# Kernel tuning notes

Measured on AMD Instinct MI355X. Metric: run time of the kernel, lower is better.

The kernel has to match this reference:

```python
import jax, jax.numpy as jnp
import numpy as np

NUM_AUTHOR = 16604
NUM_PAPER = 12455
NUM_NODES = NUM_AUTHOR + NUM_PAPER  # 29059
EMBED_DIM = 300
B = 32768          # batch of query nodes
E = 1048576        # total neighbor edges (avg degree 32)


def setup_inputs() -> dict:
    key = jax.random.key(0)
    k1, k2, k3, k4, k5, k6 = jax.random.split(key, 6)
    nodes = jax.random.randint(k1, (B,), 0, NUM_NODES)
    seg = jnp.sort(jax.random.randint(k2, (E,), 0, B))
    neighbors = jax.random.randint(k3, (E,), 0, NUM_NODES)
    embeddings = jax.random.normal(k4, (NUM_NODES, EMBED_DIM), dtype=jnp.float32)
    # linear1: Linear(3*300 -> 300)
    lim = 1.0 / np.sqrt(3 * EMBED_DIM)
    W1 = jax.random.uniform(k5, (EMBED_DIM, 3 * EMBED_DIM), dtype=jnp.float32, minval=-lim, maxval=lim)
    b1 = jax.random.uniform(k6, (EMBED_DIM,), dtype=jnp.float32, minval=-lim, maxval=lim)
    return {"nodes": nodes, "seg": seg, "neighbors": neighbors,
            "embeddings": embeddings, "W1": W1, "b1": b1}


def reference(nodes, seg, neighbors, embeddings, W1, b1):
    # Gather neighbor embeddings: [E, D] (dominant memory traffic)
    nb_emb = embeddings[neighbors]
    # type_1 = same node type as the query node, type_2 = the other type
    same = (neighbors < NUM_AUTHOR) == (nodes[seg] < NUM_AUTHOR)  # [E] bool
    w1 = same.astype(nb_emb.dtype)[:, None]
    w2 = 1.0 - w1
    sum1 = jax.ops.segment_sum(nb_emb * w1, seg, num_segments=B)   # [B, D]
    sum2 = jax.ops.segment_sum(nb_emb * w2, seg, num_segments=B)
    cnt1 = jax.ops.segment_sum(w1[:, 0], seg, num_segments=B)[:, None]  # [B,1]
    cnt2 = jax.ops.segment_sum(w2[:, 0], seg, num_segments=B)[:, None]
    # mean pooling; empty type falls back to ones (as in the torch code)
    t1 = jnp.where(cnt1 > 0, sum1 / jnp.maximum(cnt1, 1.0), 1.0)
    t2 = jnp.where(cnt2 > 0, sum2 / jnp.maximum(cnt2, 1.0), 1.0)
    self_f = embeddings[nodes]  # [B, D]
    combined = jnp.concatenate([self_f, t1, t2], axis=-1)  # [B, 3D]
    return combined @ W1.T + b1  # [B, D]
```

## Files before the change

### kernel.cpp

```cpp
#include <hip/hip_runtime.h>
#include <hip/hip_bf16.h>

#define NUM_AUTHOR 16604
#define EMB_D      300
#define BQ         32768
#define NEDGE      1048576
#define KPAD 960
#define NPAD 320
#define DPAD 320
#define NNODES 29059

#define SEG_BLOCKS 4096
#define PW_BLOCKS  1200
#define CE_BLOCKS  18162

typedef __attribute__((ext_vector_type(8))) short bf16x8;
typedef __attribute__((ext_vector_type(4))) float f32x4;

__device__ __forceinline__ unsigned short f2bf(float f) {
  unsigned int u = __float_as_uint(f);
  u += 0x7fffu + ((u >> 16) & 1u);
  return (unsigned short)(u >> 16);
}

__device__ __forceinline__ void async_copy16(const void* g, void* lds_base) {
  __builtin_amdgcn_global_load_lds(
      (const __attribute__((address_space(1))) unsigned int*)g,
      (__attribute__((address_space(3))) unsigned int*)lds_base, 16, 0, 0);
}

__global__ void prep_all(const int* __restrict__ seg, int* __restrict__ start,
                         const float* __restrict__ W1, unsigned short* __restrict__ Wt,
                         const float* __restrict__ emb, unsigned short* __restrict__ embB) {
  int blk = blockIdx.x;
  if (blk < SEG_BLOCKS) {
    int i = blk * 256 + threadIdx.x;
    int s = seg[i];
    int prev = (i == 0) ? -1 : seg[i - 1];
    if (s != prev) {
      for (int b = prev + 1; b <= s; ++b) start[b] = i;
    }
    if (i == NEDGE - 1) {
      for (int b = s + 1; b <= BQ; ++b) start[b] = NEDGE;
    }
  } else if (blk < SEG_BLOCKS + PW_BLOCKS) {
    int i = (blk - SEG_BLOCKS) * 256 + threadIdx.x;
    int n = i / KPAD, k = i % KPAD;
    int sec = k / 320, kk = k % 320;
    unsigned short v = 0;
    if (n < 300 && kk < 300) v = f2bf(W1[n * 900 + sec * 300 + kk]);
    Wt[i] = v;
  } else {
    int i = (blk - SEG_BLOCKS - PW_BLOCKS) * 256 + threadIdx.x;
    if (i >= NNODES * (DPAD / 2)) return;
    int r = i / (DPAD / 2), cu = i % (DPAD / 2);
    int c = 2 * cu;
    unsigned int lo = 0, hi = 0;
    if (c < EMB_D)     lo = f2bf(emb[(size_t)r * EMB_D + c]);
    if (c + 1 < EMB_D) hi = f2bf(emb[(size_t)r * EMB_D + c + 1]);
    ((unsigned int*)embB)[i] = lo | (hi << 16);
  }
}

__device__ __forceinline__ void accum8(uint4 p, int bit,
                                       float2* atot, float2* a1) {
  unsigned int pk[4] = {p.x, p.y, p.z, p.w};
  float2 v[4];
  #pragma unroll
  for (int k = 0; k < 4; ++k) {
    v[k].x = __uint_as_float(pk[k] << 16);
    v[k].y = __uint_as_float(pk[k] & 0xffff0000u);
  }
  #pragma unroll
  for (int k = 0; k < 4; ++k) {
    atot[k].x += v[k].x; atot[k].y += v[k].y;
  }
  if (__builtin_amdgcn_readfirstlane(bit)) {
    #pragma unroll
    for (int k = 0; k < 4; ++k) {
      a1[k].x += v[k].x; a1[k].y += v[k].y;
    }
  }
}

__global__ __launch_bounds__(128) void pool(
    const int* __restrict__ nodes, const int* __restrict__ neighbors,
    const int* __restrict__ start, const unsigned short* __restrict__ embB,
    unsigned short* __restrict__ comb) {
  int b = blockIdx.x * 2 + (threadIdx.x >> 6);
  int l = threadIdx.x & 63;
  int s0 = start[b], s1 = start[b + 1];
  int node = nodes[b];
  int qa = (node < NUM_AUTHOR) ? 1 : 0;
  bool act = (l < 40);
  const unsigned short* ep = embB + 8 * l;

  float2 atot[4], a1[4];
  #pragma unroll
  for (int k = 0; k < 4; ++k) {
    atot[k] = make_float2(0.f, 0.f);
    a1[k]   = make_float2(0.f, 0.f);
  }
  int c1 = 0;
  int rem = s1 - s0;

  for (int base = 0; base < rem; base += 64) {
    int cl = min(64, rem - base);
    int idx = neighbors[s0 + base + min(l, cl - 1)];
    int same = (((idx < NUM_AUTHOR) ? 1 : 0) == qa) ? 1 : 0;
    unsigned long long bal = __ballot(same != 0);
    unsigned long long msk = (cl >= 64) ? ~0ull : ((1ull << cl) - 1ull);
    c1 += __popcll(bal & msk);
    int off = idx * DPAD;

    int j2 = 0;
    for (; j2 + 8 <= cl; j2 += 8) {
      int o[8];
      #pragma unroll
      for (int q = 0; q < 8; ++q) o[q] = __shfl(off, j2 + q);
      if (act) {
        uint4 p[8];
        #pragma unroll
        for (int q = 0; q < 8; ++q) p[q] = *(const uint4*)(ep + o[q]);
        #pragma unroll
        for (int q = 0; q < 8; ++q)
          accum8(p[q], (int)((bal >> (j2 + q)) & 1), atot, a1);
      }
    }
    for (; j2 < cl; ++j2) {
      int o = __shfl(off, j2);
      if (act) {
        uint4 p = *(const uint4*)(ep + o);
        accum8(p, (int)((bal >> j2) & 1), atot, a1);
      }
    }
  }

  int c2 = rem - c1;
  if (!act) return;

  uint4 selfv = *(const uint4*)(embB + (size_t)node * DPAD + 8 * l);
  float r1 = c1 ? 1.0f / (float)c1 : 0.0f;
  float r2 = c2 ? 1.0f / (float)c2 : 0.0f;
  unsigned int o1[4], o2[4];
  #pragma unroll
  for (int k = 0; k < 4; ++k) {
    float t1lo = c1 ? a1[k].x * r1 : 1.0f;
    float t1hi = c1 ? a1[k].y * r1 : 1.0f;
    float t2lo = c2 ? (atot[k].x - a1[k].x) * r2 : 1.0f;
    float t2hi = c2 ? (atot[k].y - a1[k].y) * r2 : 1.0f;
    o1[k] = (unsigned int)f2bf(t1lo) | ((unsigned int)f2bf(t1hi) << 16);
    o2[k] = (unsigned int)f2bf(t2lo) | ((unsigned int)f2bf(t2hi) << 16);
  }
  uint4* crow = (uint4*)(comb + (size_t)b * KPAD);
  crow[l]      = selfv;
  crow[40 + l] = (uint4){o1[0], o1[1], o1[2], o1[3]};
  crow[80 + l] = (uint4){o2[0], o2[1], o2[2], o2[3]};
}

__global__ __launch_bounds__(256) void gemm(
    const unsigned short* __restrict__ A,
    const unsigned short* __restrict__ Bt,
    const float* __restrict__ b1,
    float* __restrict__ out) {
  __shared__ __align__(16) unsigned short As[64 * 96];
  __shared__ __align__(16) unsigned short Bs[160 * 96];

  int tid  = threadIdx.x;
  int lane = tid & 63;
  int w    = tid >> 6;
  int quad = lane >> 4;
  int l16  = lane & 15;
  int bm = blockIdx.x >> 1;
  int bn = blockIdx.x & 1;
  int wm = w >> 1, wn = w & 1;

  f32x4 acc[2][5];
  for (int i = 0; i < 2; ++i)
    for (int j = 0; j < 5; ++j)
      acc[i][j] = (f32x4){0.f, 0.f, 0.f, 0.f};

  const size_t Abase = (size_t)bm * 64 * KPAD;
  const size_t Bbase = (size_t)bn * 160 * KPAD;

  for (int kt = 0; kt < KPAD / 96; ++kt) {
    int k0 = kt * 96;
    __syncthreads();
    for (int c = w; c < 12; c += 4) {
      int flat = c * 64 + lane;
      int row = flat / 12, kq = flat % 12;
      const unsigned short* g = A + Abase + (size_t)row * KPAD + k0 + kq * 8;
      async_copy16(g, (char*)As + c * 1024);
    }
    for (int c = w; c < 30; c += 4) {
      int flat = c * 64 + lane;
      int nrow = flat / 12, kq = flat % 12;
      const unsigned short* g = Bt + Bbase + (size_t)nrow * KPAD + k0 + kq * 8;
      async_copy16(g, (char*)Bs + c * 1024);
    }
    __syncthreads();

    #pragma unroll
    for (int ks = 0; ks < 3; ++ks) {
      bf16x8 af[2], bf[5];
      for (int rt = 0; rt < 2; ++rt)
        af[rt] = *(const bf16x8*)&As[(wm * 32 + rt * 16 + l16) * 96 + ks * 32 + quad * 8];
      for (int ct = 0; ct < 5; ++ct)
        bf[ct] = *(const bf16x8*)&Bs[(wn * 80 + ct * 16 + l16) * 96 + ks * 32 + quad * 8];
      for (int rt = 0; rt < 2; ++rt)
        for (int ct = 0; ct < 5; ++ct)
          acc[rt][ct] = __builtin_amdgcn_mfma_f32_16x16x32_bf16(
              af[rt], bf[ct], acc[rt][ct], 0, 0, 0);
    }
  }

  int m0 = bm * 64 + wm * 32;
  int n0 = bn * 160 + wn * 80;
  for (int ct = 0; ct < 5; ++ct) {
    int n = n0 + ct * 16 + l16;
    if (n >= 300) continue;
    float bias = b1[n];
    for (int rt = 0; rt < 2; ++rt) {
      int m = m0 + rt * 16 + quad * 4;
      for (int r = 0; r < 4; ++r)
        out[(size_t)(m + r) * 300 + n] = acc[rt][ct][r] + bias;
    }
  }
}

__global__ __launch_bounds__(128) void pool_f32(
    const int* __restrict__ nodes, const int* __restrict__ neighbors,
    const int* __restrict__ start, const float* __restrict__ emb,
    unsigned short* __restrict__ comb) {
  int b = blockIdx.x;
  int t = threadIdx.x;
  if (t >= 80) return;
  int s0 = start[b], s1 = start[b + 1];
  int node = nodes[b];
  int qa = (node < NUM_AUTHOR) ? 1 : 0;
  bool act = (t < 75);
  float a1x = 0.f, a1y = 0.f, a1z = 0.f, a1w = 0.f;
  float a2x = 0.f, a2y = 0.f, a2z = 0.f, a2w = 0.f;
  int c1 = 0;
  #pragma unroll 2
  for (int j = s0; j < s1; ++j) {
    int nb = neighbors[j];
    int fl = (((nb < NUM_AUTHOR) ? 1 : 0) == qa) ? 1 : 0;
    c1 += fl;
    if (act) {
      const float4 v = *(const float4*)(emb + (size_t)nb * EMB_D + 4 * t);
      float w = fl ? 1.0f : 0.0f;
      float u = 1.0f - w;
      a1x += w * v.x; a1y += w * v.y; a1z += w * v.z; a1w += w * v.w;
      a2x += u * v.x; a2y += u * v.y; a2z += u * v.z; a2w += u * v.w;
    }
  }
  int c2 = (s1 - s0) - c1;
  unsigned int ps0 = 0, ps1 = 0, p10 = 0, p11 = 0, p20 = 0, p21 = 0;
  if (act) {
    const float4 sv = *(const float4*)(emb + (size_t)node * EMB_D + 4 * t);
    float r1 = c1 ? 1.0f / (float)c1 : 0.0f;
    float r2 = c2 ? 1.0f / (float)c2 : 0.0f;
    float t1x = c1 ? a1x * r1 : 1.0f, t1y = c1 ? a1y * r1 : 1.0f;
    float t1z = c1 ? a1z * r1 : 1.0f, t1w = c1 ? a1w * r1 : 1.0f;
    float t2x = c2 ? a2x * r2 : 1.0f, t2y = c2 ? a2y * r2 : 1.0f;
    float t2z = c2 ? a2z * r2 : 1.0f, t2w = c2 ? a2w * r2 : 1.0f;
    ps0 = (unsigned int)f2bf(sv.x) | ((unsigned int)f2bf(sv.y) << 16);
    ps1 = (unsigned int)f2bf(sv.z) | ((unsigned int)f2bf(sv.w) << 16);
    p10 = (unsigned int)f2bf(t1x) | ((unsigned int)f2bf(t1y) << 16);
    p11 = (unsigned int)f2bf(t1z) | ((unsigned int)f2bf(t1w) << 16);
    p20 = (unsigned int)f2bf(t2x) | ((unsigned int)f2bf(t2y) << 16);
    p21 = (unsigned int)f2bf(t2z) | ((unsigned int)f2bf(t2w) << 16);
  }
  unsigned int* crow = (unsigned int*)(comb + (size_t)b * KPAD);
  crow[2 * t]       = ps0;  crow[2 * t + 1]       = ps1;
  crow[160 + 2 * t] = p10;  crow[160 + 2 * t + 1] = p11;
  crow[320 + 2 * t] = p20;  crow[320 + 2 * t + 1] = p21;
}

__global__ void seg_bounds_only(const int* __restrict__ seg, int* __restrict__ start) {
  int i = blockIdx.x * 256 + threadIdx.x;
  if (i >= NEDGE) return;
  int s = seg[i];
  int prev = (i == 0) ? -1 : seg[i - 1];
  if (s != prev) for (int b = prev + 1; b <= s; ++b) start[b] = i;
  if (i == NEDGE - 1) for (int b = s + 1; b <= BQ; ++b) start[b] = NEDGE;
}
__global__ void prep_w_only(const float* __restrict__ W1, unsigned short* __restrict__ Wt) {
  int i = blockIdx.x * 256 + threadIdx.x;
  if (i >= NPAD * KPAD) return;
  int n = i / KPAD, k = i % KPAD;
  int sec = k / 320, kk = k % 320;
  unsigned short v = 0;
  if (n < 300 && kk < 300) v = f2bf(W1[n * 900 + sec * 300 + kk]);
  Wt[i] = v;
}

extern "C" void kernel_launch(void* const* d_in, const int* in_sizes, int n_in,
                              void* d_out, int out_size, void* d_ws, size_t ws_size,
                              hipStream_t stream) {
  const int* nodes     = (const int*)d_in[0];
  const int* seg       = (const int*)d_in[1];
  const int* neighbors = (const int*)d_in[2];
  const float* emb     = (const float*)d_in[3];
  const float* W1      = (const float*)d_in[4];
  const float* b1      = (const float*)d_in[5];
  float* out           = (float*)d_out;

  char* ws = (char*)d_ws;
  int* start           = (int*)ws;
  unsigned short* Wt   = (unsigned short*)(ws + 131584);
  unsigned short* comb = (unsigned short*)(ws + 746496);
  unsigned short* embB = (unsigned short*)(ws + 63661056);
  const size_t WS_NEEDED = 82258816;

  if (ws_size >= WS_NEEDED) {
    prep_all<<<SEG_BLOCKS + PW_BLOCKS + CE_BLOCKS, 256, 0, stream>>>(
        seg, start, W1, Wt, emb, embB);
    pool<<<BQ / 2, 128, 0, stream>>>(nodes, neighbors, start, embB, comb);
  } else {
    seg_bounds_only<<<SEG_BLOCKS, 256, 0, stream>>>(seg, start);
    prep_w_only<<<PW_BLOCKS, 256, 0, stream>>>(W1, Wt);
    pool_f32<<<BQ, 128, 0, stream>>>(nodes, neighbors, start, emb, comb);
  }
  gemm<<<1024, 256, 0, stream>>>(comb, Wt, b1, out);
}
```

Baseline: 230.5 us.

## Double-buffer GEMM LDS tiles with XOR swizzle and vectorize embedding bf16 conversion

```diff
diff --git a/kernel.cpp b/kernel.cpp
--- a/kernel.cpp
+++ b/kernel.cpp
@@ -12,7 +12,7 @@
 
 #define SEG_BLOCKS 4096
 #define PW_BLOCKS  1200
-#define CE_BLOCKS  18162
+#define CE_BLOCKS  4541
 
 typedef __attribute__((ext_vector_type(8))) short bf16x8;
 typedef __attribute__((ext_vector_type(4))) float f32x4;
@@ -52,13 +52,23 @@
     Wt[i] = v;
   } else {
     int i = (blk - SEG_BLOCKS - PW_BLOCKS) * 256 + threadIdx.x;
-    if (i >= NNODES * (DPAD / 2)) return;
-    int r = i / (DPAD / 2), cu = i % (DPAD / 2);
-    int c = 2 * cu;
-    unsigned int lo = 0, hi = 0;
-    if (c < EMB_D)     lo = f2bf(emb[(size_t)r * EMB_D + c]);
-    if (c + 1 < EMB_D) hi = f2bf(emb[(size_t)r * EMB_D + c + 1]);
-    ((unsigned int*)embB)[i] = lo | (hi << 16);
+    if (i >= NNODES * 40) return;
+    int r = i / 40, q = i % 40;
+    const float* src = emb + (size_t)r * EMB_D + q * 8;
+    unsigned int u[4] = {0, 0, 0, 0};
+    if (q < 37) {
+      float4 v0 = *(const float4*)src;
+      float4 v1 = *(const float4*)(src + 4);
+      u[0] = (unsigned int)f2bf(v0.x) | ((unsigned int)f2bf(v0.y) << 16);
+      u[1] = (unsigned int)f2bf(v0.z) | ((unsigned int)f2bf(v0.w) << 16);
+      u[2] = (unsigned int)f2bf(v1.x) | ((unsigned int)f2bf(v1.y) << 16);
+      u[3] = (unsigned int)f2bf(v1.z) | ((unsigned int)f2bf(v1.w) << 16);
+    } else if (q == 37) {
+      float4 v0 = *(const float4*)src;
+      u[0] = (unsigned int)f2bf(v0.x) | ((unsigned int)f2bf(v0.y) << 16);
+      u[1] = (unsigned int)f2bf(v0.z) | ((unsigned int)f2bf(v0.w) << 16);
+    }
+    ((uint4*)embB)[i] = (uint4){u[0], u[1], u[2], u[3]};
   }
 }
 
@@ -163,8 +173,8 @@
     const unsigned short* __restrict__ Bt,
     const float* __restrict__ b1,
     float* __restrict__ out) {
-  __shared__ __align__(16) unsigned short As[64 * 96];
-  __shared__ __align__(16) unsigned short Bs[160 * 96];
+  __shared__ __align__(16) unsigned short As[2][64 * 64];
+  __shared__ __align__(16) unsigned short Bs[2][160 * 64];
 
   int tid  = threadIdx.x;
   int lane = tid & 63;
@@ -183,31 +193,46 @@
   const size_t Abase = (size_t)bm * 64 * KPAD;
   const size_t Bbase = (size_t)bn * 160 * KPAD;
 
-  for (int kt = 0; kt < KPAD / 96; ++kt) {
-    int k0 = kt * 96;
+  auto stage = [&](int kt, int buf) {
+    int k0 = kt * 64;
+    for (int c = w; c < 8; c += 4) {
+      int flat = c * 64 + lane;
+      int row = flat >> 3, g = flat & 7;
+      int kq = g ^ (row & 7);
+      const unsigned short* gp = A + Abase + (size_t)row * KPAD + k0 + kq * 8;
+      async_copy16(gp, (char*)&As[buf][0] + c * 1024);
+    }
+    for (int c = w; c < 20; c += 4) {
+      int flat = c * 64 + lane;
+      int row = flat >> 3, g = flat & 7;
+      int kq = g ^ (row & 7);
+      const unsigned short* gp = Bt + Bbase + (size_t)row * KPAD + k0 + kq * 8;
+      async_copy16(gp, (char*)&Bs[buf][0] + c * 1024);
+    }
+  };
+
+  stage(0, 0);
+  for (int kt = 0; kt < KPAD / 64; ++kt) {
+    int cur = kt & 1;
     __syncthreads();
-    for (int c = w; c < 12; c += 4) {
-      int flat = c * 64 + lane;
-      int row = flat / 12, kq = flat % 12;
-      const unsigned short* g = A + Abase + (size_t)row * KPAD + k0 + kq * 8;
-      async_copy16(g, (char*)As + c * 1024);
-    }
-    for (int c = w; c < 30; c += 4) {
-      int flat = c * 64 + lane;
-      int nrow = flat / 12, kq = flat % 12;
-      const unsigned short* g = Bt + Bbase + (size_t)nrow * KPAD + k0 + kq * 8;
-      async_copy16(g, (char*)Bs + c * 1024);
-    }
-    __syncthreads();
-
+    if (kt + 1 < KPAD / 64) stage(kt + 1, cur ^ 1);
     #pragma unroll
-    for (int ks = 0; ks < 3; ++ks) {
+    for (int ks = 0; ks < 2; ++ks) {
+      int gi = ks * 4 + quad;
       bf16x8 af[2], bf[5];
+      #pragma unroll
+      for (int rt = 0; rt < 2; ++rt) {
+        int row = wm * 32 + rt * 16 + l16;
+        af[rt] = *(const bf16x8*)&As[cur][row * 64 + ((gi ^ (row & 7)) << 3)];
+      }
+      #pragma unroll
+      for (int ct = 0; ct < 5; ++ct) {
+        int row = wn * 80 + ct * 16 + l16;
+        bf[ct] = *(const bf16x8*)&Bs[cur][row * 64 + ((gi ^ (row & 7)) << 3)];
+      }
+      #pragma unroll
       for (int rt = 0; rt < 2; ++rt)
-        af[rt] = *(const bf16x8*)&As[(wm * 32 + rt * 16 + l16) * 96 + ks * 32 + quad * 8];
-      for (int ct = 0; ct < 5; ++ct)
-        bf[ct] = *(const bf16x8*)&Bs[(wn * 80 + ct * 16 + l16) * 96 + ks * 32 + quad * 8];
-      for (int rt = 0; rt < 2; ++rt)
+        #pragma unroll
         for (int ct = 0; ct < 5; ++ct)
           acc[rt][ct] = __builtin_amdgcn_mfma_f32_16x16x32_bf16(
               af[rt], bf[ct], acc[rt][ct], 0, 0, 0);
```

After: 227.8 us. No clear change (-1.2%).
